# Optimization experiments

Hardware: AMD Instinct MI355X
Metric: run time of the kernel (lower is better)

## Reference

```python
import jax, jax.numpy as jnp
import numpy as np

H = 1024   # hidden_size
A = 16     # number_ab (branches)
O = 4      # num_outputs per branch
B = 4096   # batch
P = 2048   # number of selected rows
EPS = 1e-5


def setup_inputs() -> dict:
    key = jax.random.key(0)
    ks = jax.random.split(key, 12)
    s = 0.02  # weight init scale
    inp = {
        "X": jax.random.normal(ks[0], (B, H), jnp.float32),
        "X1": jax.random.normal(ks[1], (B, H), jnp.float32),
        # stacked per-branch parameters (batched over antibody axis A)
        "W1": jax.random.normal(ks[2], (A, H, H), jnp.float32) * s,
        "b1": jnp.zeros((A, H), jnp.float32),
        "W2": jax.random.normal(ks[3], (A, H, H), jnp.float32) * s,
        "b2": jnp.zeros((A, H), jnp.float32),
        "W3": jax.random.normal(ks[4], (A, H, H), jnp.float32) * s,
        "b3": jnp.zeros((A, H), jnp.float32),
        "gamma": jnp.ones((A, H), jnp.float32),
        "beta": jnp.zeros((A, H), jnp.float32),
        "W4": jax.random.normal(ks[5], (A, H, O), jnp.float32) * s,
        "b4": jnp.zeros((A, O), jnp.float32),
        "positions_y": jax.random.randint(ks[6], (P,), 0, B, jnp.int32),
    }
    return inp


def reference(X, X1, W1, b1, W2, b2, W3, b3, gamma, beta, W4, b4, positions_y):
    # z = l1(X) + l2(X1) per branch, batched over A: [B, A, H]
    z = (jnp.einsum('bh,aho->bao', X, W1) + b1
         + jnp.einsum('bh,aho->bao', X1, W2) + b2)
    # mlm: Linear -> ReLU -> LayerNorm -> Linear
    h = jax.nn.relu(jnp.einsum('bah,aho->bao', z, W3) + b3)  # [B, A, H]
    mu = jnp.mean(h, axis=-1, keepdims=True)
    var = jnp.var(h, axis=-1, keepdims=True)  # biased, matches nn.LayerNorm
    hn = (h - mu) / jnp.sqrt(var + EPS) * gamma + beta
    y = jnp.einsum('bah,aho->bao', hn, W4) + b4  # [B, A, O]
    # torch.cat along dim 1 over branches -> [B, A*O]
    Y = y.reshape(B, A * O)
    return Y[positions_y]
```

## Files before the change

### kernel.cpp

```cpp
#include <hip/hip_runtime.h>
#include <hip/hip_bf16.h>

using bf16 = __hip_bfloat16;
typedef __bf16 v8bf __attribute__((ext_vector_type(8)));
typedef float v4f __attribute__((ext_vector_type(4)));

#define H_ 1024
#define A_ 16
#define O_ 4
#define B_ 4096
#define P_ 2048
#define EPS_ 1e-5f

__device__ __forceinline__ void gl_lds16(const void* g, void* l) {
    __builtin_amdgcn_global_load_lds(
        (const __attribute__((address_space(1))) void*)g,
        (__attribute__((address_space(3))) void*)l, 16, 0, 0);
}

__global__ void addbias_k(const float* __restrict__ b1, const float* __restrict__ b2,
                          float* __restrict__ b12, int n) {
    int i = blockIdx.x * 256 + threadIdx.x;
    if (i < n) b12[i] = b1[i] + b2[i];
}

__global__ __launch_bounds__(256) void gather_k(const float* __restrict__ X,
                                                const float* __restrict__ X1,
                                                const int* __restrict__ pos,
                                                bf16* __restrict__ XX) {
    int p = blockIdx.x;
    int row = pos[p];
    const float4* x  = (const float4*)(X  + (size_t)row * H_);
    const float4* x1 = (const float4*)(X1 + (size_t)row * H_);
    bf16* o = XX + (size_t)p * (2 * H_);
    int i = threadIdx.x;
    float4 v = x[i];
    o[i * 4 + 0] = __float2bfloat16(v.x);
    o[i * 4 + 1] = __float2bfloat16(v.y);
    o[i * 4 + 2] = __float2bfloat16(v.z);
    o[i * 4 + 3] = __float2bfloat16(v.w);
    float4 w = x1[i];
    o[H_ + i * 4 + 0] = __float2bfloat16(w.x);
    o[H_ + i * 4 + 1] = __float2bfloat16(w.y);
    o[H_ + i * 4 + 2] = __float2bfloat16(w.z);
    o[H_ + i * 4 + 3] = __float2bfloat16(w.w);
}

__global__ __launch_bounds__(256) void transpose_conv_k(const float* __restrict__ src,
                                                        bf16* __restrict__ dst,
                                                        int K, int N, int dstK, int kOff) {
    __shared__ float tile[32][33];
    int a = blockIdx.z;
    int k0 = blockIdx.x * 32;
    int n0 = blockIdx.y * 32;
    const float* s = src + (size_t)a * K * N;
    int tc = threadIdx.x & 31;
    int tr = threadIdx.x >> 5;
#pragma unroll
    for (int r = 0; r < 32; r += 8)
        tile[tr + r][tc] = s[(size_t)(k0 + tr + r) * N + n0 + tc];
    __syncthreads();
    bf16* d = dst + (size_t)a * N * dstK;
#pragma unroll
    for (int r = 0; r < 32; r += 8) {
        int n = n0 + tr + r;
        int k = k0 + tc;
        d[(size_t)n * dstK + kOff + k] = __float2bfloat16(tile[tc][tr + r]);
    }
}

template <bool RELU>
__global__ __launch_bounds__(256) void gemm_bt(const bf16* __restrict__ Amat, size_t aStrideA,
                                               const bf16* __restrict__ Bt,
                                               const float* __restrict__ bias,
                                               bf16* __restrict__ C,
                                               int M, int N, int K) {
    constexpr int BM = 128, BN = 128, BK = 32;
    __shared__ __align__(16) unsigned short As[BM * BK];
    __shared__ __align__(16) unsigned short Bs[BN * BK];

    const int a = blockIdx.z;
    const bf16* Ab = Amat + (size_t)a * aStrideA;
    const bf16* Bb = Bt + (size_t)a * (size_t)N * K;
    const int bm = blockIdx.x, bn = blockIdx.y;
    const int tid = threadIdx.x;
    const int lane = tid & 63;
    const int wave = tid >> 6;
    const int wm = (wave & 1) * 64;
    const int wn = (wave >> 1) * 64;

    v4f acc[4][4];
#pragma unroll
    for (int i = 0; i < 4; i++)
#pragma unroll
        for (int j = 0; j < 4; j++) acc[i][j] = (v4f){0.f, 0.f, 0.f, 0.f};

    const int r0 = tid >> 2;
    const int c0 = (tid & 3) * 8;
    const bf16* agBase = Ab + (size_t)(bm * BM + r0) * K + c0;
    const bf16* bgBase = Bb + (size_t)(bn * BN + r0) * K + c0;
    unsigned short* aLds0 = As + wave * 512;
    unsigned short* aLds1 = As + 2048 + wave * 512;
    unsigned short* bLds0 = Bs + wave * 512;
    unsigned short* bLds1 = Bs + 2048 + wave * 512;
    const size_t rowSkip = (size_t)64 * K;

    const int kq = (lane >> 4) * 8;
    const int lr = lane & 15;

    for (int k0 = 0; k0 < K; k0 += BK) {
        gl_lds16(agBase + k0, aLds0);
        gl_lds16(agBase + k0 + rowSkip, aLds1);
        gl_lds16(bgBase + k0, bLds0);
        gl_lds16(bgBase + k0 + rowSkip, bLds1);
        __syncthreads();
        v8bf af[4], bfr[4];
#pragma unroll
        for (int mi = 0; mi < 4; mi++)
            af[mi] = *(const v8bf*)(As + (wm + mi * 16 + lr) * BK + kq);
#pragma unroll
        for (int ni = 0; ni < 4; ni++)
            bfr[ni] = *(const v8bf*)(Bs + (wn + ni * 16 + lr) * BK + kq);
#pragma unroll
        for (int mi = 0; mi < 4; mi++)
#pragma unroll
            for (int ni = 0; ni < 4; ni++)
                acc[mi][ni] = __builtin_amdgcn_mfma_f32_16x16x32_bf16(af[mi], bfr[ni],
                                                                      acc[mi][ni], 0, 0, 0);
        __syncthreads();
    }

    const int lq = lane >> 4;
    bf16* Cb = C + (size_t)a * M * N;
#pragma unroll
    for (int ni = 0; ni < 4; ni++) {
        const int col = bn * BN + wn + ni * 16 + lr;
        const float bv = bias[(size_t)a * N + col];
#pragma unroll
        for (int mi = 0; mi < 4; mi++) {
            const int row0 = bm * BM + wm + mi * 16 + lq * 4;
#pragma unroll
            for (int rg = 0; rg < 4; rg++) {
                float v = acc[mi][ni][rg] + bv;
                if (RELU) v = v > 0.f ? v : 0.f;
                Cb[(size_t)(row0 + rg) * N + col] = __float2bfloat16(v);
            }
        }
    }
}

__global__ __launch_bounds__(256) void ln_head_k(const bf16* __restrict__ Hb,
                                                 const float* __restrict__ gamma,
                                                 const float* __restrict__ beta,
                                                 const float* __restrict__ W4,
                                                 const float* __restrict__ b4,
                                                 float* __restrict__ out) {
    int w = blockIdx.x * 4 + (threadIdx.x >> 6);
    int lane = threadIdx.x & 63;
    int a = w >> 11;
    int p = w & (P_ - 1);
    const bf16* hrow = Hb + ((size_t)a * P_ + p) * H_;
    float hv[16];
    float s = 0.f, ss = 0.f;
#pragma unroll
    for (int i = 0; i < 16; i++) {
        float v = __bfloat162float(hrow[lane + i * 64]);
        hv[i] = v;
        s += v;
        ss += v * v;
    }
#pragma unroll
    for (int off = 32; off; off >>= 1) {
        s += __shfl_xor(s, off);
        ss += __shfl_xor(ss, off);
    }
    float mu = s * (1.f / H_);
    float var = ss * (1.f / H_) - mu * mu;
    float rstd = rsqrtf(var + EPS_);
    const float* g = gamma + (size_t)a * H_;
    const float* be = beta + (size_t)a * H_;
    const float4* w4 = (const float4*)(W4 + (size_t)a * H_ * O_);
    float a0 = 0.f, a1 = 0.f, a2 = 0.f, a3 = 0.f;
#pragma unroll
    for (int i = 0; i < 16; i++) {
        int k = lane + i * 64;
        float hn = (hv[i] - mu) * rstd * g[k] + be[k];
        float4 wv = w4[k];
        a0 += hn * wv.x;
        a1 += hn * wv.y;
        a2 += hn * wv.z;
        a3 += hn * wv.w;
    }
#pragma unroll
    for (int off = 32; off; off >>= 1) {
        a0 += __shfl_xor(a0, off);
        a1 += __shfl_xor(a1, off);
        a2 += __shfl_xor(a2, off);
        a3 += __shfl_xor(a3, off);
    }
    if (lane < 4) {
        float v = (lane == 0 ? a0 : lane == 1 ? a1 : lane == 2 ? a2 : a3) + b4[a * O_ + lane];
        out[(size_t)p * (A_ * O_) + a * O_ + lane] = v;
    }
}

extern "C" void kernel_launch(void* const* d_in, const int* in_sizes, int n_in,
                              void* d_out, int out_size, void* d_ws, size_t ws_size,
                              hipStream_t stream) {
    const float* X     = (const float*)d_in[0];
    const float* X1    = (const float*)d_in[1];
    const float* W1    = (const float*)d_in[2];
    const float* b1    = (const float*)d_in[3];
    const float* W2    = (const float*)d_in[4];
    const float* b2    = (const float*)d_in[5];
    const float* W3    = (const float*)d_in[6];
    const float* b3    = (const float*)d_in[7];
    const float* gamma = (const float*)d_in[8];
    const float* beta  = (const float*)d_in[9];
    const float* W4    = (const float*)d_in[10];
    const float* b4    = (const float*)d_in[11];
    const int* pos     = (const int*)d_in[12];
    float* out = (float*)d_out;

    char* ws = (char*)d_ws;
    bf16* XX   = (bf16*)(ws);
    bf16* Z    = (bf16*)(ws + ((size_t)8 << 20));
    bf16* WT3  = (bf16*)(ws + ((size_t)72 << 20));
    bf16* WT12 = (bf16*)(ws + ((size_t)104 << 20));
    float* b12 = (float*)(ws + ((size_t)168 << 20));
    bf16* Hb   = WT12;

    addbias_k<<<(A_ * H_ + 255) / 256, 256, 0, stream>>>(b1, b2, b12, A_ * H_);
    gather_k<<<P_, 256, 0, stream>>>(X, X1, pos, XX);
    dim3 tgrid(H_ / 32, H_ / 32, A_);
    transpose_conv_k<<<tgrid, 256, 0, stream>>>(W1, WT12, H_, H_, 2 * H_, 0);
    transpose_conv_k<<<tgrid, 256, 0, stream>>>(W2, WT12, H_, H_, 2 * H_, H_);
    transpose_conv_k<<<tgrid, 256, 0, stream>>>(W3, WT3, H_, H_, H_, 0);

    dim3 g1(P_ / 128, H_ / 128, A_);
    gemm_bt<false><<<g1, 256, 0, stream>>>(XX, 0, WT12, b12, Z, P_, H_, 2 * H_);
    gemm_bt<true><<<g1, 256, 0, stream>>>(Z, (size_t)P_ * H_, WT3, b3, Hb, P_, H_, H_);

    ln_head_k<<<P_ * A_ / 4, 256, 0, stream>>>(Hb, gamma, beta, W4, b4, out);
}
```

Measured before the change: 551.0 us.

## Fuse weight transposes into one vectorized kernel and swizzle GEMM LDS layout

Merges the three per-matrix fp32→bf16 transpose launches into a single kernel with 64x64 tiles, float4 loads and 16-byte bf16 stores. The gather kernel also writes packed bf16 quads instead of scalars. In the GEMM, the k-chunk each thread loads into LDS is XOR-swizzled by row, and the fragment reads use the matching swizzle, to cut LDS bank conflicts. The risks are that the swizzle must match exactly between the global-to-LDS writes and the fragment reads, and that the larger transpose tile uses more shared memory per block.

```diff
diff --git a/kernel.cpp b/kernel.cpp
--- a/kernel.cpp
+++ b/kernel.cpp
@@ -35,37 +35,53 @@
     bf16* o = XX + (size_t)p * (2 * H_);
     int i = threadIdx.x;
     float4 v = x[i];
-    o[i * 4 + 0] = __float2bfloat16(v.x);
-    o[i * 4 + 1] = __float2bfloat16(v.y);
-    o[i * 4 + 2] = __float2bfloat16(v.z);
-    o[i * 4 + 3] = __float2bfloat16(v.w);
+    __align__(8) bf16 t[4];
+    t[0] = __float2bfloat16(v.x); t[1] = __float2bfloat16(v.y);
+    t[2] = __float2bfloat16(v.z); t[3] = __float2bfloat16(v.w);
+    *(uint2*)(o + i * 4) = *(const uint2*)t;
     float4 w = x1[i];
-    o[H_ + i * 4 + 0] = __float2bfloat16(w.x);
-    o[H_ + i * 4 + 1] = __float2bfloat16(w.y);
-    o[H_ + i * 4 + 2] = __float2bfloat16(w.z);
-    o[H_ + i * 4 + 3] = __float2bfloat16(w.w);
-}
-
-__global__ __launch_bounds__(256) void transpose_conv_k(const float* __restrict__ src,
-                                                        bf16* __restrict__ dst,
-                                                        int K, int N, int dstK, int kOff) {
-    __shared__ float tile[32][33];
-    int a = blockIdx.z;
-    int k0 = blockIdx.x * 32;
-    int n0 = blockIdx.y * 32;
-    const float* s = src + (size_t)a * K * N;
-    int tc = threadIdx.x & 31;
-    int tr = threadIdx.x >> 5;
-#pragma unroll
-    for (int r = 0; r < 32; r += 8)
-        tile[tr + r][tc] = s[(size_t)(k0 + tr + r) * N + n0 + tc];
+    t[0] = __float2bfloat16(w.x); t[1] = __float2bfloat16(w.y);
+    t[2] = __float2bfloat16(w.z); t[3] = __float2bfloat16(w.w);
+    *(uint2*)(o + H_ + i * 4) = *(const uint2*)t;
+}
+
+__global__ __launch_bounds__(256) void transpose3_k(const float* __restrict__ W1s,
+                                                    const float* __restrict__ W2s,
+                                                    const float* __restrict__ W3s,
+                                                    bf16* __restrict__ WT12,
+                                                    bf16* __restrict__ WT3) {
+    __shared__ float tile[64][65];
+    const int which = blockIdx.z >> 4;
+    const int a = blockIdx.z & 15;
+    const float* src = (which == 0) ? W1s : (which == 1) ? W2s : W3s;
+    bf16* dstBase = (which == 2) ? WT3 : WT12;
+    const int dstK = (which == 2) ? H_ : 2 * H_;
+    const int kOff = (which == 1) ? H_ : 0;
+
+    const int k0 = blockIdx.x * 64;
+    const int n0 = blockIdx.y * 64;
+    const float* s = src + (size_t)a * H_ * H_;
+    const int tc = threadIdx.x & 15;
+    const int tr = threadIdx.x >> 4;
+#pragma unroll
+    for (int r = 0; r < 64; r += 16) {
+        float4 v = *(const float4*)(s + (size_t)(k0 + tr + r) * H_ + n0 + tc * 4);
+        tile[tr + r][tc * 4 + 0] = v.x;
+        tile[tr + r][tc * 4 + 1] = v.y;
+        tile[tr + r][tc * 4 + 2] = v.z;
+        tile[tr + r][tc * 4 + 3] = v.w;
+    }
     __syncthreads();
-    bf16* d = dst + (size_t)a * N * dstK;
-#pragma unroll
-    for (int r = 0; r < 32; r += 8) {
-        int n = n0 + tr + r;
-        int k = k0 + tc;
-        d[(size_t)n * dstK + kOff + k] = __float2bfloat16(tile[tc][tr + r]);
+    bf16* d = dstBase + (size_t)a * H_ * dstK + kOff;
+    const int wc = threadIdx.x & 7;
+    const int wr = threadIdx.x >> 3;
+#pragma unroll
+    for (int r = 0; r < 64; r += 32) {
+        const int n = wr + r;
+        __align__(16) bf16 tmp[8];
+#pragma unroll
+        for (int j = 0; j < 8; j++) tmp[j] = __float2bfloat16(tile[wc * 8 + j][n]);
+        *(uint4*)(d + (size_t)(n0 + n) * dstK + k0 + wc * 8) = *(const uint4*)tmp;
     }
 }
 
@@ -96,17 +112,18 @@
         for (int j = 0; j < 4; j++) acc[i][j] = (v4f){0.f, 0.f, 0.f, 0.f};
 
     const int r0 = tid >> 2;
-    const int c0 = (tid & 3) * 8;
-    const bf16* agBase = Ab + (size_t)(bm * BM + r0) * K + c0;
-    const bf16* bgBase = Bb + (size_t)(bn * BN + r0) * K + c0;
+    const int cs = (((tid & 3) ^ ((r0 >> 1) & 3))) * 8;
+    const bf16* agBase = Ab + (size_t)(bm * BM + r0) * K + cs;
+    const bf16* bgBase = Bb + (size_t)(bn * BN + r0) * K + cs;
     unsigned short* aLds0 = As + wave * 512;
     unsigned short* aLds1 = As + 2048 + wave * 512;
     unsigned short* bLds0 = Bs + wave * 512;
     unsigned short* bLds1 = Bs + 2048 + wave * 512;
     const size_t rowSkip = (size_t)64 * K;
 
-    const int kq = (lane >> 4) * 8;
     const int lr = lane & 15;
+    const int q = lane >> 4;
+    const int kq = (q ^ ((lr >> 1) & 3)) * 8;
 
     for (int k0 = 0; k0 < K; k0 += BK) {
         gl_lds16(agBase + k0, aLds0);
@@ -232,10 +249,8 @@
 
     addbias_k<<<(A_ * H_ + 255) / 256, 256, 0, stream>>>(b1, b2, b12, A_ * H_);
     gather_k<<<P_, 256, 0, stream>>>(X, X1, pos, XX);
-    dim3 tgrid(H_ / 32, H_ / 32, A_);
-    transpose_conv_k<<<tgrid, 256, 0, stream>>>(W1, WT12, H_, H_, 2 * H_, 0);
-    transpose_conv_k<<<tgrid, 256, 0, stream>>>(W2, WT12, H_, H_, 2 * H_, H_);
-    transpose_conv_k<<<tgrid, 256, 0, stream>>>(W3, WT3, H_, H_, H_, 0);
+    dim3 tgrid(H_ / 64, H_ / 64, 3 * A_);
+    transpose3_k<<<tgrid, 256, 0, stream>>>(W1, W2, W3, WT12, WT3);
 
     dim3 g1(P_ / 128, H_ / 128, A_);
     gemm_bt<false><<<g1, 256, 0, stream>>>(XX, 0, WT12, b12, Z, P_, H_, 2 * H_);
```

Measured after the change: 549.9 us. Within noise of the previous version (-0.2%).
